# Kernel optimization log

Measured on AMD Instinct MI355X. Metric: run time of the kernel, lower is better.

Reference implementation:

```python
import jax, jax.numpy as jnp
import numpy as np

B, T, NMELS = 2, 2048, 64
D, H, DH, M, L = 256, 4, 64, 384, 4
FF2 = 2 * 4 * D  # GLU doubles the 4*dim hidden


def _layernorm(x, g, b):
    m = x.mean(-1, keepdims=True)
    v = ((x - m) ** 2).mean(-1, keepdims=True)
    return (x - m) * jax.lax.rsqrt(v + 1e-5) * g + b


def _conv(h, w, groups=1, pad='VALID'):
    return jax.lax.conv_general_dilated(h, w, (1, 1), pad, feature_group_count=groups,
                                        dimension_numbers=('NCHW', 'OIHW', 'NCHW'))


def _bn(h, g, b, m, v):
    return (h - m[:, None, None]) * jax.lax.rsqrt(v[:, None, None] + 1e-5) * g[:, None, None] + b[:, None, None]


def setup_inputs():
    key = jax.random.key(0)
    ks = jax.random.split(key, 40)
    def n(i, shape, s):
        return (jax.random.normal(ks[i], shape) * s).astype(jnp.float32)
    z = lambda shape: jnp.zeros(shape, jnp.float32)
    o = lambda shape: jnp.ones(shape, jnp.float32)
    return dict(
        x=n(0, (B, T, NMELS), 1.0),
        conv0_w=n(1, (4, 1, 1, 1), 0.5),
        dw1_w=n(2, (4, 1, 3, 3), 0.3), dw1_b=z(4),
        pw1_w=n(3, (D // 2, 4, 1, 1), 0.5), pw1_b=z(D // 2),
        bn1_g=o(D // 2), bn1_b=z(D // 2), bn1_m=n(4, (D // 2,), 0.05), bn1_v=o(D // 2),
        dw2_w=n(5, (D // 2, 1, 3, 3), 0.3), dw2_b=z(D // 2),
        pw2_w=n(6, (D, D // 2, 1, 1), 0.1), pw2_b=z(D),
        bn2_g=o(D), bn2_b=z(D), bn2_m=n(7, (D,), 0.05), bn2_v=o(D),
        proj_w=n(8, (D, D), 0.06), proj_b=z(D),
        ln0_g=o(D), ln0_b=z(D),
        pos_emb=n(9, (1, T, D), 0.02),
        ln1_g=o((L, D)), ln1_b=z((L, D)),
        wq=n(10, (L, D, D), 0.06), bq=z((L, D)),
        wk=n(11, (L, D, D), 0.06), bk=z((L, D)),
        wv=n(12, (L, D, D), 0.06), bv=z((L, D)),
        wo=n(13, (L, D, D), 0.06), bo=z((L, D)),
        proj_mat=n(14, (L, M, DH), 1.0),
        ln2_g=o((L, D)), ln2_b=z((L, D)),
        ffw1=n(15, (L, D, FF2), 0.06), ffb1=z((L, FF2)),
        ffw2=n(16, (L, FF2 // 2, D), 0.03), ffb2=z((L, D)),
        clf_w1=n(17, (D, D // 2), 0.06), clf_b1=z(D // 2),
        clf_ln_g=o(D // 2), clf_ln_b=z(D // 2),
        clf_w2=n(18, (D // 2, 1), 0.09), clf_b2=z(1),
    )


def reference(x, conv0_w, dw1_w, dw1_b, pw1_w, pw1_b, bn1_g, bn1_b, bn1_m, bn1_v,
              dw2_w, dw2_b, pw2_w, pw2_b, bn2_g, bn2_b, bn2_m, bn2_v,
              proj_w, proj_b, ln0_g, ln0_b, pos_emb,
              ln1_g, ln1_b, wq, bq, wk, bk, wv, bv, wo, bo, proj_mat,
              ln2_g, ln2_b, ffw1, ffb1, ffw2, ffb2,
              clf_w1, clf_b1, clf_ln_g, clf_ln_b, clf_w2, clf_b2):
    pad1 = ((1, 1), (1, 1))
    # conv frontend: [B,T,n_mels] -> [B,1,n_mels,T]
    h = x.transpose(0, 2, 1)[:, None]
    h = _conv(h, conv0_w)
    h = _conv(h, dw1_w, groups=4, pad=pad1) + dw1_b[:, None, None]
    h = _conv(h, pw1_w) + pw1_b[:, None, None]
    h = jax.nn.relu(_bn(h, bn1_g, bn1_b, bn1_m, bn1_v))
    h = _conv(h, dw2_w, groups=D // 2, pad=pad1) + dw2_b[:, None, None]
    h = _conv(h, pw2_w) + pw2_b[:, None, None]
    h = jax.nn.relu(_bn(h, bn2_g, bn2_b, bn2_m, bn2_v))
    h = h.mean(axis=2).transpose(0, 2, 1)  # [B,T,D]
    h = h @ proj_w + proj_b
    h = _layernorm(h, ln0_g, ln0_b) + pos_emb[:, :h.shape[1]]
    # reversible Performer: streams x1 (attn) / x2 (ff), combined by sum
    x1, x2 = h, h
    dn = DH ** -0.25
    for l in range(L):
        a = _layernorm(x2, ln1_g[l], ln1_b[l])
        Bsz, N, _ = a.shape
        q = (a @ wq[l] + bq[l]).reshape(Bsz, N, H, DH).transpose(0, 2, 1, 3)
        k = (a @ wk[l] + bk[l]).reshape(Bsz, N, H, DH).transpose(0, 2, 1, 3)
        v = (a @ wv[l] + bv[l]).reshape(Bsz, N, H, DH).transpose(0, 2, 1, 3)
        # FAVOR+ generalized (ReLU) kernel feature maps, eps=1e-3
        qf = jax.nn.relu(jnp.einsum('bhnd,jd->bhnj', dn * q, proj_mat[l])) + 1e-3
        kf = jax.nn.relu(jnp.einsum('bhnd,jd->bhnj', dn * k, proj_mat[l])) + 1e-3
        d_inv = 1.0 / jnp.einsum('bhnj,bhj->bhn', qf, kf.sum(axis=2))
        ctx = jnp.einsum('bhnj,bhnd->bhjd', kf, v)
        o = jnp.einsum('bhjd,bhnj,bhn->bhnd', ctx, qf, d_inv)
        o = o.transpose(0, 2, 1, 3).reshape(Bsz, N, D)
        x1 = x1 + (o @ wo[l] + bo[l])
        f = _layernorm(x1, ln2_g[l], ln2_b[l])
        u1, u2 = jnp.split(f @ ffw1[l] + ffb1[l], 2, axis=-1)
        x2 = x2 + (jax.nn.gelu(u1, approximate=False) * u2) @ ffw2[l] + ffb2[l]
    h = x1 + x2
    c = jax.nn.relu(_layernorm(h @ clf_w1 + clf_b1, clf_ln_g, clf_ln_b))
    return (c @ clf_w2 + clf_b2)[..., 0]
```

## Files before the change

### kernel.cpp

```cpp
#include <hip/hip_runtime.h>
#include <hip/hip_bf16.h>
#include <math.h>

using bf16 = __hip_bfloat16;
typedef __attribute__((ext_vector_type(8))) short short8;
typedef __attribute__((ext_vector_type(4))) float f32x4;

__device__ __forceinline__ float tof(float x) { return x; }
__device__ __forceinline__ float tof(bf16 x) { return __bfloat162float(x); }
__device__ __forceinline__ float b2f(unsigned short u) {
  union { float f; unsigned int i; } c; c.i = ((unsigned int)u) << 16; return c.f;
}
__device__ __forceinline__ unsigned short f2bu(float v) {
  bf16 h = __float2bfloat16(v);
  return *(unsigned short*)&h;
}
__device__ __forceinline__ void sto1(float* p, float v) { *p = v; }
__device__ __forceinline__ void sto1(bf16* p, float v) { *p = __float2bfloat16(v); }

__device__ __forceinline__ float gelu_exact(float x) {
  return 0.5f * x * (1.f + erff(x * 0.70710678118654752f));
}

__device__ __forceinline__ void llds16(const bf16* g, short* l) {
  __builtin_amdgcn_global_load_lds((const __attribute__((address_space(1))) void*)g,
                                   (__attribute__((address_space(3))) void*)l, 16, 0, 0);
}

__global__ __launch_bounds__(256) void pack_qkv_kernel(
    const float* __restrict__ wq, const float* __restrict__ wk,
    const float* __restrict__ wv, bf16* __restrict__ out)
{
  int idx = blockIdx.x * 256 + threadIdx.x;
  int k = idx & 255;
  int nl = idx >> 8;
  int n = nl % 768, l = nl / 768;
  const float* src = (n < 256) ? wq : (n < 512 ? wk : wv);
  out[idx] = __float2bfloat16(src[(long)l * 65536 + k * 256 + (n & 255)]);
}

__global__ __launch_bounds__(256) void pack_qkvbias_kernel(
    const float* __restrict__ bq, const float* __restrict__ bk,
    const float* __restrict__ bv, float* __restrict__ out)
{
  int i = blockIdx.x * 256 + threadIdx.x;
  if (i >= 3072) return;
  int n = i % 768, l = i / 768;
  const float* src = (n < 256) ? bq : (n < 512 ? bk : bv);
  out[i] = src[l * 256 + (n & 255)];
}

__global__ __launch_bounds__(256) void tconv_kernel(
    const float* __restrict__ in, bf16* __restrict__ out,
    int K, int N, long sin, long sout)
{
  int l = blockIdx.z;
  int idx = blockIdx.x * 256 + threadIdx.x;
  int k = idx % K, n = idx / K;
  out[l * sout + idx] = __float2bfloat16(in[l * sin + (long)k * N + n]);
}

__global__ __launch_bounds__(256) void f2b_kernel(
    const float* __restrict__ in, bf16* __restrict__ out, int n)
{
  int i = blockIdx.x * 256 + threadIdx.x;
  if (i < n) out[i] = __float2bfloat16(in[i]);
}

__global__ __launch_bounds__(256) void zero4_kernel(float* __restrict__ p) {
  int i = (blockIdx.x * 256 + threadIdx.x) * 4;
  float4 z; z.x = 0.f; z.y = 0.f; z.z = 0.f; z.w = 0.f;
  *(float4*)&p[i] = z;
}

__global__ __launch_bounds__(256) void sumb_kernel(
    const float* __restrict__ a, const float* __restrict__ b, bf16* __restrict__ o)
{
  int i = (blockIdx.x * 256 + threadIdx.x) * 4;
  float4 x = *(const float4*)&a[i];
  float4 y = *(const float4*)&b[i];
  ushort4 p;
  p.x = f2bu(x.x + y.x); p.y = f2bu(x.y + y.y);
  p.z = f2bu(x.z + y.z); p.w = f2bu(x.w + y.w);
  *(ushort4*)((unsigned short*)o + i) = p;
}

__global__ __launch_bounds__(256) void front1_kernel(
    const float* __restrict__ x, const float* __restrict__ c0w,
    const float* __restrict__ d1w, const float* __restrict__ d1b,
    const float* __restrict__ p1w, const float* __restrict__ p1b,
    const float* __restrict__ g1, const float* __restrict__ b1,
    const float* __restrict__ m1, const float* __restrict__ v1,
    bf16* __restrict__ A1)
{
  __shared__ float sd[256];
  __shared__ float spw[512];
  __shared__ float ss[128], st[128], sb[128];
  int tid = threadIdx.x;
  int bt = blockIdx.x;
  int b = bt >> 11, t = bt & 2047;
  if (tid < 128) {
    float s = g1[tid] * rsqrtf(v1[tid] + 1e-5f);
    ss[tid] = s;
    st[tid] = b1[tid] - m1[tid] * s;
    sb[tid] = p1b[tid];
#pragma unroll
    for (int c = 0; c < 4; ++c) spw[c * 128 + tid] = p1w[tid * 4 + c];
  }
  {
    int c = tid >> 6, f = tid & 63;
    float cw = c0w[c];
    float acc = d1b[c];
#pragma unroll
    for (int kh = 0; kh < 3; ++kh) {
      int fi = f + kh - 1;
      if (fi < 0 || fi >= 64) continue;
#pragma unroll
      for (int kw = 0; kw < 3; ++kw) {
        int ti = t + kw - 1;
        if (ti < 0 || ti >= 2048) continue;
        acc += d1w[c * 9 + kh * 3 + kw] * cw * x[((long)b * 2048 + ti) * 64 + fi];
      }
    }
    sd[c * 64 + f] = acc;
  }
  __syncthreads();
  long ob = (long)bt * 8192;
  for (int it = 0; it < 32; ++it) {
    int o = it * 256 + tid;
    int f = o >> 7, ci = o & 127;
    float pre = sb[ci];
#pragma unroll
    for (int c = 0; c < 4; ++c) pre = fmaf(spw[c * 128 + ci], sd[c * 64 + f], pre);
    A1[ob + o] = __float2bfloat16(fmaxf(fmaf(ss[ci], pre, st[ci]), 0.f));
  }
}

__global__ __launch_bounds__(256) void convtail_kernel(
    const bf16* __restrict__ A1, const float* __restrict__ w,
    const float* __restrict__ wb, const bf16* __restrict__ w2b,
    const float* __restrict__ pb, const float* __restrict__ g2,
    const float* __restrict__ b2, const float* __restrict__ m2,
    const float* __restrict__ v2, bf16* __restrict__ hconvb)
{
  __shared__ short dw2s[64 * 136];
  __shared__ short Bs[64 * 136];
  __shared__ float red[1024];
  __shared__ float ssc[64], ssh[64];
  int tid = threadIdx.x;
  int lane = tid & 63, wv = tid >> 6;
  int quad = lane >> 4, l15 = lane & 15;
  int rw = (wv >> 1) * 32, cw = (wv & 1) * 32;
  int bt = blockIdx.x, b = bt >> 11, t = bt & 2047;
  int ci4 = (tid & 31) * 4;
  float wreg[9][4], breg[4];
#pragma unroll
  for (int c = 0; c < 4; ++c) {
    breg[c] = wb[ci4 + c];
#pragma unroll
    for (int kk = 0; kk < 9; ++kk) wreg[kk][c] = w[(ci4 + c) * 9 + kk];
  }
  const unsigned short* A1u = (const unsigned short*)A1;
  for (int pass = 0; pass < 8; ++pass) {
    int f = pass * 8 + (tid >> 5);
    float a0 = breg[0], a1 = breg[1], a2 = breg[2], a3 = breg[3];
#pragma unroll
    for (int kh = 0; kh < 3; ++kh) {
      int fi = f + kh - 1;
      if (fi < 0 || fi >= 64) continue;
#pragma unroll
      for (int kw = 0; kw < 3; ++kw) {
        int ti = t + kw - 1;
        if (ti < 0 || ti >= 2048) continue;
        ushort4 u = *(const ushort4*)&A1u[(((long)b * 2048 + ti) * 64 + fi) * 128 + ci4];
        int kk = kh * 3 + kw;
        a0 = fmaf(wreg[kk][0], b2f(u.x), a0);
        a1 = fmaf(wreg[kk][1], b2f(u.y), a1);
        a2 = fmaf(wreg[kk][2], b2f(u.z), a2);
        a3 = fmaf(wreg[kk][3], b2f(u.w), a3);
      }
    }
    ushort4 p; p.x = f2bu(a0); p.y = f2bu(a1); p.z = f2bu(a2); p.w = f2bu(a3);
    *(ushort4*)&dw2s[f * 136 + ci4] = p;
  }
  for (int ct = 0; ct < 4; ++ct) {
    int co0 = ct * 64;
    __syncthreads();
    for (int l2 = 0; l2 < 4; ++l2) {
      int idx = l2 * 256 + tid;
      int row = idx >> 4, koff = (idx & 15) * 8;
      *(short8*)&Bs[row * 136 + koff] =
          *(const short8*)&w2b[(long)(co0 + row) * 128 + koff];
    }
    if (tid < 64) {
      int co = co0 + tid;
      float s = g2[co] * rsqrtf(v2[co] + 1e-5f);
      ssc[tid] = s;
      ssh[tid] = b2[co] - m2[co] * s + s * pb[co];
    }
    __syncthreads();
    f32x4 zv = {0.f, 0.f, 0.f, 0.f};
    f32x4 acc[2][2] = {{zv, zv}, {zv, zv}};
#pragma unroll
    for (int kc = 0; kc < 4; ++kc) {
      short8 a0 = *(const short8*)&dw2s[(rw + l15) * 136 + kc * 32 + quad * 8];
      short8 a1 = *(const short8*)&dw2s[(rw + 16 + l15) * 136 + kc * 32 + quad * 8];
      short8 b0 = *(const short8*)&Bs[(cw + l15) * 136 + kc * 32 + quad * 8];
      short8 b1 = *(const short8*)&Bs[(cw + 16 + l15) * 136 + kc * 32 + quad * 8];
      acc[0][0] = __builtin_amdgcn_mfma_f32_16x16x32_bf16(a0, b0, acc[0][0], 0, 0, 0);
      acc[0][1] = __builtin_amdgcn_mfma_f32_16x16x32_bf16(a0, b1, acc[0][1], 0, 0, 0);
      acc[1][0] = __builtin_amdgcn_mfma_f32_16x16x32_bf16(a1, b0, acc[1][0], 0, 0, 0);
      acc[1][1] = __builtin_amdgcn_mfma_f32_16x16x32_bf16(a1, b1, acc[1][1], 0, 0, 0);
    }
#pragma unroll
    for (int mi = 0; mi < 2; ++mi)
#pragma unroll
      for (int nj = 0; nj < 2; ++nj) {
        int colg = cw + nj * 16 + l15;
        float s = ssc[colg], sh = ssh[colg];
        float sum = 0.f;
#pragma unroll
        for (int r = 0; r < 4; ++r) sum += fmaxf(fmaf(s, acc[mi][nj][r], sh), 0.f);
        int rowgroup = (wv >> 1) * 8 + mi * 4 + quad;
        red[rowgroup * 64 + colg] = sum;
      }
    __syncthreads();
    if (tid < 64) {
      float s = 0.f;
#pragma unroll
      for (int r = 0; r < 16; ++r) s += red[r * 64 + tid];
      hconvb[(long)bt * 256 + co0 + tid] = __float2bfloat16(s * (1.f / 64.f));
    }
  }
}

template <typename CTy, int EPI>
__global__ __launch_bounds__(256) void mgemm_kernel(
    const bf16* __restrict__ A, const bf16* __restrict__ Bt,
    const float* __restrict__ bias, const float* __restrict__ res,
    const float* __restrict__ rowsc, CTy* __restrict__ C, bf16* __restrict__ C2,
    int K, int lda, int ldbt, int ldc,
    long sAb, long sAh, long sBb, long sBh, long sCb, long sCh,
    long sRb, long sRh, int Hdiv, float alpha)
{
  __shared__ short As[4096];
  __shared__ short Bs[4096];
  __shared__ short Bs2[(EPI == 8) ? 4096 : 8];
  int tid = threadIdx.x;
  int lane = tid & 63, w = tid >> 6;
  int quad = lane >> 4, l15 = lane & 15;
  int rw = (w >> 1) * 32, cw = (w & 1) * 32;
  int r0 = blockIdx.x * 64, n0 = blockIdx.y * 64;
  int zb = blockIdx.z / Hdiv, zh = blockIdx.z % Hdiv;
  A += zb * sAb + zh * sAh;
  Bt += zb * sBb + zh * sBh;
  C += zb * sCb + zh * sCh;
  if (res) res += zb * sCb + zh * sCh;
  const float* rsp = (EPI == 3) ? rowsc + zb * sRb + zh * sRh : nullptr;
  f32x4 zv = {0.f, 0.f, 0.f, 0.f};
  f32x4 acc[2][2] = {{zv, zv}, {zv, zv}};
  f32x4 acc2[2][2] = {{zv, zv}, {zv, zv}};
  const bf16* Ag = A + (long)(r0 + (tid >> 2)) * lda + ((tid & 3) * 8);
  const bf16* Bg = Bt + (long)(n0 + (tid >> 2)) * ldbt + ((tid & 3) * 8);
  const bf16* Bg2 = (EPI == 8) ? Bg + sRb : nullptr;
  short* Asd = &As[tid * 8];
  short* Bsd = &Bs[tid * 8];
  short* Bs2d = &Bs2[(EPI == 8) ? tid * 8 : 0];
  for (int k0 = 0; k0 < K; k0 += 64) {
    if (k0) __syncthreads();
    llds16(Ag + k0, Asd);
    llds16(Ag + k0 + 32, Asd + 2048);
    llds16(Bg + k0, Bsd);
    llds16(Bg + k0 + 32, Bsd + 2048);
    if constexpr (EPI == 8) {
      llds16(Bg2 + k0, Bs2d);
      llds16(Bg2 + k0 + 32, Bs2d + 2048);
    }
    __syncthreads();
#pragma unroll
    for (int c = 0; c < 2; ++c) {
      short8 a0 = *(const short8*)&As[c * 2048 + (rw + l15) * 32 + quad * 8];
      short8 a1 = *(const short8*)&As[c * 2048 + (rw + 16 + l15) * 32 + quad * 8];
      short8 b0 = *(const short8*)&Bs[c * 2048 + (cw + l15) * 32 + quad * 8];
      short8 b1 = *(const short8*)&Bs[c * 2048 + (cw + 16 + l15) * 32 + quad * 8];
      acc[0][0] = __builtin_amdgcn_mfma_f32_16x16x32_bf16(a0, b0, acc[0][0], 0, 0, 0);
      acc[0][1] = __builtin_amdgcn_mfma_f32_16x16x32_bf16(a0, b1, acc[0][1], 0, 0, 0);
      acc[1][0] = __builtin_amdgcn_mfma_f32_16x16x32_bf16(a1, b0, acc[1][0], 0, 0, 0);
      acc[1][1] = __builtin_amdgcn_mfma_f32_16x16x32_bf16(a1, b1, acc[1][1], 0, 0, 0);
      if constexpr (EPI == 8) {
        short8 c0 = *(const short8*)&Bs2[c * 2048 + (cw + l15) * 32 + quad * 8];
        short8 c1 = *(const short8*)&Bs2[c * 2048 + (cw + 16 + l15) * 32 + quad * 8];
        acc2[0][0] = __builtin_amdgcn_mfma_f32_16x16x32_bf16(a0, c0, acc2[0][0], 0, 0, 0);
        acc2[0][1] = __builtin_amdgcn_mfma_f32_16x16x32_bf16(a0, c1, acc2[0][1], 0, 0, 0);
        acc2[1][0] = __builtin_amdgcn_mfma_f32_16x16x32_bf16(a1, c0, acc2[1][0], 0, 0, 0);
        acc2[1][1] = __builtin_amdgcn_mfma_f32_16x16x32_bf16(a1, c1, acc2[1][1], 0, 0, 0);
      }
    }
  }
#pragma unroll
  for (int mi = 0; mi < 2; ++mi)
#pragma unroll
    for (int nj = 0; nj < 2; ++nj) {
      int colg = n0 + cw + nj * 16 + l15;
      float bv_ = bias ? bias[colg] : 0.f;
      float bv2 = (EPI == 8) ? bias[colg + 1024] : 0.f;
      int rbase = r0 + rw + mi * 16 + quad * 4;
      float ov[4];
#pragma unroll
      for (int r = 0; r < 4; ++r) {
        float v = acc[mi][nj][r];
        if constexpr (EPI == 0 || EPI == 5) {
          v += bv_;
        } else if constexpr (EPI == 1) {
          v += bv_ + res[(long)(rbase + r) * ldc + colg];
        } else if constexpr (EPI == 2 || EPI == 6) {
          v = fmaxf(v * alpha, 0.f) + 1e-3f;
        } else if constexpr (EPI == 3) {
          v *= rsp[rbase + r];
        } else if constexpr (EPI == 4) {
          v = gelu_exact(v + bv_) * res[(long)(rbase + r) * ldc + colg];
        } else if constexpr (EPI == 8) {
          v = gelu_exact(v + bv_) * (acc2[mi][nj][r] + bv2);
        }
        ov[r] = v;
      }
      if constexpr (EPI == 6) {
        ushort4 p;
        p.x = f2bu(ov[0]); p.y = f2bu(ov[1]); p.z = f2bu(ov[2]); p.w = f2bu(ov[3]);
        *(ushort4*)((unsigned short*)C + (long)colg * ldc + rbase) = p;
      } else if constexpr (EPI == 5) {
        if (colg < 512) {
#pragma unroll
          for (int r = 0; r < 4; ++r) sto1(&C[(long)(rbase + r) * ldc + colg], ov[r]);
        } else {
          int bb = rbase >> 11, t0 = rbase & 2047;
          long off = (((long)bb * 4 + ((colg - 512) >> 6)) * 64 + (colg & 63)) * 2048 + t0;
          ushort4 p;
          p.x = f2bu(ov[0]); p.y = f2bu(ov[1]); p.z = f2bu(ov[2]); p.w = f2bu(ov[3]);
          *(ushort4*)((unsigned short*)C2 + off) = p;
        }
      } else if constexpr (EPI == 7) {
#pragma unroll
        for (int r = 0; r < 4; ++r)
          atomicAdd((float*)&C[(long)(rbase + r) * ldc + colg], ov[r]);
      } else {
#pragma unroll
        for (int r = 0; r < 4; ++r) sto1(&C[(long)(rbase + r) * ldc + colg], ov[r]);
      }
    }
  (void)alpha;
}

template <int DIM, bool RELU, bool ADDPOS, bool DUAL, typename OTy>
__global__ __launch_bounds__(256) void ln_kernel(
    const float* __restrict__ in, const float* __restrict__ g,
    const float* __restrict__ b, const float* __restrict__ pos,
    OTy* __restrict__ out0, float* __restrict__ out1)
{
  constexpr int CH = DIM / 64;
  int row = blockIdx.x * 4 + (threadIdx.x >> 6);
  int lane = threadIdx.x & 63;
  const float* rp = in + (long)row * DIM + lane * CH;
  float v[CH];
#pragma unroll
  for (int i = 0; i < CH; ++i) v[i] = rp[i];
  float s = 0.f;
#pragma unroll
  for (int i = 0; i < CH; ++i) s += v[i];
#pragma unroll
  for (int o = 32; o > 0; o >>= 1) s += __shfl_xor(s, o, 64);
  float mean = s * (1.f / DIM);
  float q = 0.f;
#pragma unroll
  for (int i = 0; i < CH; ++i) { float d = v[i] - mean; q += d * d; }
#pragma unroll
  for (int o = 32; o > 0; o >>= 1) q += __shfl_xor(q, o, 64);
  float rstd = rsqrtf(q * (1.f / DIM) + 1e-5f);
  int t = row & 2047;
#pragma unroll
  for (int i = 0; i < CH; ++i) {
    int c = lane * CH + i;
    float o = (v[i] - mean) * rstd * g[c] + b[c];
    if constexpr (ADDPOS) o += pos[(long)t * DIM + c];
    if constexpr (RELU) o = fmaxf(o, 0.f);
    sto1(&out0[(long)row * DIM + c], o);
    if constexpr (DUAL) out1[(long)row * DIM + c] = o;
  }
}

__global__ __launch_bounds__(256) void rowsum_kernel(
    const bf16* __restrict__ kfT, float* __restrict__ ksum)
{
  int z = blockIdx.x;
  int j = blockIdx.y * 4 + (threadIdx.x >> 6);
  int lane = threadIdx.x & 63;
  const short* base = (const short*)kfT + ((long)z * 384 + j) * 2048;
  float acc = 0.f;
#pragma unroll
  for (int i = 0; i < 4; ++i) {
    short8 v = *(const short8*)&base[i * 512 + lane * 8];
#pragma unroll
    for (int e = 0; e < 8; ++e) acc += b2f((unsigned short)v[e]);
  }
#pragma unroll
  for (int o = 32; o > 0; o >>= 1) acc += __shfl_xor(acc, o, 64);
  if (lane == 0) ksum[z * 384 + j] = acc;
}

__global__ __launch_bounds__(256) void dinv_kernel(
    const bf16* __restrict__ qf, const float* __restrict__ ksum,
    float* __restrict__ dinv)
{
  int z = blockIdx.x;
  int t = blockIdx.y * 4 + (threadIdx.x >> 6);
  int lane = threadIdx.x & 63;
  const bf16* qr = qf + ((long)z * 2048 + t) * 384;
  const float* ks = ksum + z * 384;
  float acc = 0.f;
#pragma unroll
  for (int i = 0; i < 6; ++i) {
    int j = lane + i * 64;
    acc = fmaf(tof(qr[j]), ks[j], acc);
  }
#pragma unroll
  for (int o = 32; o > 0; o >>= 1) acc += __shfl_xor(acc, o, 64);
  if (lane == 0) dinv[z * 2048 + t] = 1.f / acc;
}

__global__ __launch_bounds__(256) void clf2_kernel(
    const float* __restrict__ c2, const float* __restrict__ w,
    const float* __restrict__ b, float* __restrict__ out)
{
  int row = blockIdx.x * 4 + (threadIdx.x >> 6);
  int lane = threadIdx.x & 63;
  const float* rp = c2 + (long)row * 128 + lane * 2;
  float acc = rp[0] * w[lane * 2] + rp[1] * w[lane * 2 + 1];
#pragma unroll
  for (int o = 32; o > 0; o >>= 1) acc += __shfl_xor(acc, o, 64);
  if (lane == 0) out[row] = acc + b[0];
}

extern "C" void kernel_launch(void* const* d_in, const int* in_sizes, int n_in,
                              void* d_out, int out_size, void* d_ws, size_t ws_size,
                              hipStream_t stream)
{
  const float* X    = (const float*)d_in[0];
  const float* c0w  = (const float*)d_in[1];
  const float* d1w  = (const float*)d_in[2];
  const float* d1b  = (const float*)d_in[3];
  const float* p1w  = (const float*)d_in[4];
  const float* p1b  = (const float*)d_in[5];
  const float* g1   = (const float*)d_in[6];
  const float* b1   = (const float*)d_in[7];
  const float* m1   = (const float*)d_in[8];
  const float* v1   = (const float*)d_in[9];
  const float* d2w  = (const float*)d_in[10];
  const float* d2b  = (const float*)d_in[11];
  const float* p2w  = (const float*)d_in[12];
  const float* p2b  = (const float*)d_in[13];
  const float* g2   = (const float*)d_in[14];
  const float* b2   = (const float*)d_in[15];
  const float* m2   = (const float*)d_in[16];
  const float* v2   = (const float*)d_in[17];
  const float* projw= (const float*)d_in[18];
  const float* projb= (const float*)d_in[19];
  const float* ln0g = (const float*)d_in[20];
  const float* ln0b = (const float*)d_in[21];
  const float* pos  = (const float*)d_in[22];
  const float* ln1g = (const float*)d_in[23];
  const float* ln1b = (const float*)d_in[24];
  const float* wq   = (const float*)d_in[25];
  const float* bq   = (const float*)d_in[26];
  const float* wk   = (const float*)d_in[27];
  const float* bk   = (const float*)d_in[28];
  const float* wv   = (const float*)d_in[29];
  const float* bv   = (const float*)d_in[30];
  const float* wo   = (const float*)d_in[31];
  const float* bo   = (const float*)d_in[32];
  const float* pmat = (const float*)d_in[33];
  const float* ln2g = (const float*)d_in[34];
  const float* ln2b = (const float*)d_in[35];
  const float* ffw1 = (const float*)d_in[36];
  const float* ffb1 = (const float*)d_in[37];
  const float* ffw2 = (const float*)d_in[38];
  const float* ffb2 = (const float*)d_in[39];
  const float* cw1  = (const float*)d_in[40];
  const float* cb1  = (const float*)d_in[41];
  const float* clng = (const float*)d_in[42];
  const float* clnb = (const float*)d_in[43];
  const float* cw2  = (const float*)d_in[44];
  const float* cb2  = (const float*)d_in[45];
  (void)in_sizes; (void)n_in; (void)out_size; (void)ws_size;

  float* ws     = (float*)d_ws;
  float* x1     = ws;
  float* x2     = ws + 1048576;
  float* lnb32  = ws + 2097152;
  bf16*  lnb16  = (bf16*)(ws + 3145728);
  bf16*  hconvb = (bf16*)(ws + 3407872);
  bf16*  obufb  = (bf16*)(ws + 3670016);
  bf16*  qkvb   = (bf16*)(ws + 3932160);
  bf16*  vT     = (bf16*)(ws + 5505024);
  bf16*  qf     = (bf16*)(ws + 6029312);
  bf16*  kfT    = (bf16*)(ws + 9175040);
  float* ctx32  = ws + 12320768;
  float* ksum   = ws + 12517376;
  float* dinvp  = ws + 12521472;
  bf16*  ctxb   = (bf16*)(ws + 12537856);
  float* c1     = ws + 12587008;
  float* c2     = ws + 13111296;
  bf16*  gb2    = (bf16*)(ws + 16633856);
  bf16*  A1     = (bf16*)(ws + 3670016);
  bf16*  wqkv_bf= (bf16*)(ws + 20447232);
  float* qkvbias= ws + 20840448;
  bf16*  f1w_bf = (bf16*)(ws + 20843520);
  bf16*  f2w_bf = (bf16*)(ws + 21892096);
  bf16*  wo_bf  = (bf16*)(ws + 22416384);
  bf16*  pm_bf  = (bf16*)(ws + 22547456);
  bf16*  projwT = (bf16*)(ws + 22596608);
  bf16*  cw1T   = (bf16*)(ws + 22629376);
  bf16*  pw2_bf = (bf16*)(ws + 22645760);
  bf16*  sbuf   = qkvb;

  const float dn = 0.35355339059327378f;

  pack_qkv_kernel<<<3072, 256, 0, stream>>>(wq, wk, wv, wqkv_bf);
  pack_qkvbias_kernel<<<12, 256, 0, stream>>>(bq, bk, bv, qkvbias);
  tconv_kernel<<<dim3(2048, 1, 4), 256, 0, stream>>>(ffw1, f1w_bf, 256, 2048, 524288, 524288);
  tconv_kernel<<<dim3(1024, 1, 4), 256, 0, stream>>>(ffw2, f2w_bf, 1024, 256, 262144, 262144);
  tconv_kernel<<<dim3(256, 1, 4), 256, 0, stream>>>(wo, wo_bf, 256, 256, 65536, 65536);
  tconv_kernel<<<dim3(256, 1, 1), 256, 0, stream>>>(projw, projwT, 256, 256, 65536, 65536);
  tconv_kernel<<<dim3(128, 1, 1), 256, 0, stream>>>(cw1, cw1T, 256, 128, 32768, 32768);
  f2b_kernel<<<384, 256, 0, stream>>>(pmat, pm_bf, 98304);
  f2b_kernel<<<128, 256, 0, stream>>>(p2w, pw2_bf, 32768);

  front1_kernel<<<4096, 256, 0, stream>>>(X, c0w, d1w, d1b, p1w, p1b, g1, b1, m1, v1, A1);
  convtail_kernel<<<4096, 256, 0, stream>>>(A1, d2w, d2b, pw2_bf, p2b, g2, b2, m2, v2, hconvb);

  mgemm_kernel<float, 0><<<dim3(64, 4, 1), 256, 0, stream>>>(
      hconvb, projwT, projb, nullptr, nullptr, lnb32, nullptr,
      256, 256, 256, 256, 0, 0, 0, 0, 0, 0, 0, 0, 1, 1.f);
  ln_kernel<256, false, true, true, float><<<1024, 256, 0, stream>>>(
      lnb32, ln0g, ln0b, pos, x1, x2);

  for (int l = 0; l < 4; ++l) {
    const bf16* wqkv_l = wqkv_bf + (size_t)l * 196608;
    const float* qb_l  = qkvbias + l * 768;
    const bf16* pm_l   = pm_bf + (size_t)l * 24576;
    const bf16* wo_l   = wo_bf + (size_t)l * 65536;
    const float* bov   = bo + l * 256;
    const bf16* f1w_l  = f1w_bf + (size_t)l * 524288;
    const float* f1b_l = ffb1 + l * 2048;
    const bf16* f2w_l  = f2w_bf + (size_t)l * 262144;
    const float* f2b_l = ffb2 + l * 256;

    ln_kernel<256, false, false, false, bf16><<<1024, 256, 0, stream>>>(
        x2, ln1g + l * 256, ln1b + l * 256, nullptr, lnb16, nullptr);
    mgemm_kernel<bf16, 5><<<dim3(64, 12, 1), 256, 0, stream>>>(
        lnb16, wqkv_l, qb_l, nullptr, nullptr, qkvb, vT,
        256, 256, 256, 768, 0, 0, 0, 0, 0, 0, 0, 0, 1, 1.f);
    mgemm_kernel<bf16, 2><<<dim3(32, 6, 8), 256, 0, stream>>>(
        qkvb, pm_l, nullptr, nullptr, nullptr, qf, nullptr,
        64, 768, 64, 384, 1572864, 64, 0, 0, 3145728, 786432, 0, 0, 4, dn);
    mgemm_kernel<bf16, 6><<<dim3(32, 6, 8), 256, 0, stream>>>(
        qkvb + 256, pm_l, nullptr, nullptr, nullptr, kfT, nullptr,
        64, 768, 64, 2048, 1572864, 64, 0, 0, 6291456, 1572864, 0, 0, 4, dn);
    rowsum_kernel<<<dim3(8, 96), 256, 0, stream>>>(kfT, ksum);
    dinv_kernel<<<dim3(8, 512), 256, 0, stream>>>(qf, ksum, dinvp);
    zero4_kernel<<<192, 256, 0, stream>>>(ctx32);
    mgemm_kernel<float, 7><<<dim3(1, 6, 64), 256, 0, stream>>>(
        vT, kfT, nullptr, nullptr, nullptr, ctx32, nullptr,
        256, 2048, 2048, 384, 131072, 256, 786432, 256, 24576, 0, 0, 0, 8, 1.f);
    f2b_kernel<<<768, 256, 0, stream>>>(ctx32, ctxb, 196608);
    mgemm_kernel<bf16, 3><<<dim3(32, 1, 8), 256, 0, stream>>>(
        qf, ctxb, nullptr, nullptr, dinvp, obufb, nullptr,
        384, 384, 384, 256, 3145728, 786432, 98304, 24576, 524288, 64, 8192, 2048, 4, 1.f);
    mgemm_kernel<float, 1><<<dim3(64, 4, 1), 256, 0, stream>>>(
        obufb, wo_l, bov, x1, nullptr, x1, nullptr,
        256, 256, 256, 256, 0, 0, 0, 0, 0, 0, 0, 0, 1, 1.f);
    ln_kernel<256, false, false, false, bf16><<<1024, 256, 0, stream>>>(
        x1, ln2g + l * 256, ln2b + l * 256, nullptr, lnb16, nullptr);
    mgemm_kernel<bf16, 8><<<dim3(64, 16, 1), 256, 0, stream>>>(
        lnb16, f1w_l, f1b_l, nullptr, nullptr, gb2, nullptr,
        256, 256, 256, 1024, 0, 0, 0, 0, 0, 0, 262144, 0, 1, 1.f);
    mgemm_kernel<float, 1><<<dim3(64, 4, 1), 256, 0, stream>>>(
        gb2, f2w_l, f2b_l, x2, nullptr, x2, nullptr,
        1024, 1024, 1024, 256, 0, 0, 0, 0, 0, 0, 0, 0, 1, 1.f);
  }

  sumb_kernel<<<1024, 256, 0, stream>>>(x1, x2, sbuf);
  mgemm_kernel<float, 0><<<dim3(64, 2, 1), 256, 0, stream>>>(
      sbuf, cw1T, cb1, nullptr, nullptr, c1, nullptr,
      256, 256, 256, 128, 0, 0, 0, 0, 0, 0, 0, 0, 1, 1.f);
  ln_kernel<128, true, false, false, float><<<1024, 256, 0, stream>>>(
      c1, clng, clnb, nullptr, c2, nullptr);
  clf2_kernel<<<1024, 256, 0, stream>>>(c2, cw2, cb2, (float*)d_out);
}
```

Baseline: 680.9 us.

## Fuse FAVOR+ q/k feature maps with key-sum and widen convtail depthwise vectors

The separate q and k feature-map GEMM launches and the rowsum kernel are replaced by a single favor_kernel. It computes both maps over a doubled z grid and accumulates the key sums with atomics, which assumes the widened zero kernel also clears ksum. The convtail depthwise stage now handles 8 channels per thread with 16-byte loads and stores, and gets a launch-bounds occupancy hint. This cuts launches and the re-read of kfT, at the cost of float atomics with nondeterministic ordering and higher register use in convtail.

```diff
diff --git a/kernel.cpp b/kernel.cpp
--- a/kernel.cpp
+++ b/kernel.cpp
@@ -136,7 +136,7 @@
   }
 }
 
-__global__ __launch_bounds__(256) void convtail_kernel(
+__global__ __launch_bounds__(256, 4) void convtail_kernel(
     const bf16* __restrict__ A1, const float* __restrict__ w,
     const float* __restrict__ wb, const bf16* __restrict__ w2b,
     const float* __restrict__ pb, const float* __restrict__ g2,
@@ -152,18 +152,20 @@
   int quad = lane >> 4, l15 = lane & 15;
   int rw = (wv >> 1) * 32, cw = (wv & 1) * 32;
   int bt = blockIdx.x, b = bt >> 11, t = bt & 2047;
-  int ci4 = (tid & 31) * 4;
-  float wreg[9][4], breg[4];
-#pragma unroll
-  for (int c = 0; c < 4; ++c) {
-    breg[c] = wb[ci4 + c];
-#pragma unroll
-    for (int kk = 0; kk < 9; ++kk) wreg[kk][c] = w[(ci4 + c) * 9 + kk];
+  int ci8 = (tid & 15) * 8;
+  float wreg[9][8], breg[8];
+#pragma unroll
+  for (int c = 0; c < 8; ++c) {
+    breg[c] = wb[ci8 + c];
+#pragma unroll
+    for (int kk = 0; kk < 9; ++kk) wreg[kk][c] = w[(ci8 + c) * 9 + kk];
   }
   const unsigned short* A1u = (const unsigned short*)A1;
-  for (int pass = 0; pass < 8; ++pass) {
-    int f = pass * 8 + (tid >> 5);
-    float a0 = breg[0], a1 = breg[1], a2 = breg[2], a3 = breg[3];
+  for (int pass = 0; pass < 4; ++pass) {
+    int f = pass * 16 + (tid >> 4);
+    float a[8];
+#pragma unroll
+    for (int c = 0; c < 8; ++c) a[c] = breg[c];
 #pragma unroll
     for (int kh = 0; kh < 3; ++kh) {
       int fi = f + kh - 1;
@@ -172,16 +174,17 @@
       for (int kw = 0; kw < 3; ++kw) {
         int ti = t + kw - 1;
         if (ti < 0 || ti >= 2048) continue;
-        ushort4 u = *(const ushort4*)&A1u[(((long)b * 2048 + ti) * 64 + fi) * 128 + ci4];
+        short8 u = *(const short8*)&A1u[(((long)b * 2048 + ti) * 64 + fi) * 128 + ci8];
         int kk = kh * 3 + kw;
-        a0 = fmaf(wreg[kk][0], b2f(u.x), a0);
-        a1 = fmaf(wreg[kk][1], b2f(u.y), a1);
-        a2 = fmaf(wreg[kk][2], b2f(u.z), a2);
-        a3 = fmaf(wreg[kk][3], b2f(u.w), a3);
+#pragma unroll
+        for (int c = 0; c < 8; ++c)
+          a[c] = fmaf(wreg[kk][c], b2f((unsigned short)u[c]), a[c]);
       }
     }
-    ushort4 p; p.x = f2bu(a0); p.y = f2bu(a1); p.z = f2bu(a2); p.w = f2bu(a3);
-    *(ushort4*)&dw2s[f * 136 + ci4] = p;
+    short8 p;
+#pragma unroll
+    for (int c = 0; c < 8; ++c) p[c] = (short)f2bu(a[c]);
+    *(short8*)&dw2s[f * 136 + ci8] = p;
   }
   for (int ct = 0; ct < 4; ++ct) {
     int co0 = ct * 64;
@@ -232,6 +235,68 @@
       hconvb[(long)bt * 256 + co0 + tid] = __float2bfloat16(s * (1.f / 64.f));
     }
   }
+}
+
+__global__ __launch_bounds__(256) void favor_kernel(
+    const bf16* __restrict__ qkvb, const bf16* __restrict__ pm,
+    bf16* __restrict__ qf, bf16* __restrict__ kfT, float* __restrict__ ksum,
+    float dn)
+{
+  __shared__ short As[4096];
+  __shared__ short Bs[4096];
+  int tid = threadIdx.x;
+  int lane = tid & 63, w = tid >> 6;
+  int quad = lane >> 4, l15 = lane & 15;
+  int rw = (w >> 1) * 32, cw = (w & 1) * 32;
+  int r0 = blockIdx.x * 64, n0 = blockIdx.y * 64;
+  int z16 = blockIdx.z;
+  bool isK = z16 >= 8;
+  int z = z16 & 7, zb = z >> 2, zh = z & 3;
+  const bf16* A = qkvb + (isK ? 256 : 0) + (long)zb * 1572864 + zh * 64;
+  f32x4 zv = {0.f, 0.f, 0.f, 0.f};
+  f32x4 acc[2][2] = {{zv, zv}, {zv, zv}};
+  const bf16* Ag = A + (long)(r0 + (tid >> 2)) * 768 + ((tid & 3) * 8);
+  const bf16* Bg = pm + (long)(n0 + (tid >> 2)) * 64 + ((tid & 3) * 8);
+  llds16(Ag, &As[tid * 8]);
+  llds16(Ag + 32, &As[tid * 8 + 2048]);
+  llds16(Bg, &Bs[tid * 8]);
+  llds16(Bg + 32, &Bs[tid * 8 + 2048]);
+  __syncthreads();
+#pragma unroll
+  for (int c = 0; c < 2; ++c) {
+    short8 a0 = *(const short8*)&As[c * 2048 + (rw + l15) * 32 + quad * 8];
+    short8 a1 = *(const short8*)&As[c * 2048 + (rw + 16 + l15) * 32 + quad * 8];
+    short8 b0 = *(const short8*)&Bs[c * 2048 + (cw + l15) * 32 + quad * 8];
+    short8 b1 = *(const short8*)&Bs[c * 2048 + (cw + 16 + l15) * 32 + quad * 8];
+    acc[0][0] = __builtin_amdgcn_mfma_f32_16x16x32_bf16(a0, b0, acc[0][0], 0, 0, 0);
+    acc[0][1] = __builtin_amdgcn_mfma_f32_16x16x32_bf16(a0, b1, acc[0][1], 0, 0, 0);
+    acc[1][0] = __builtin_amdgcn_mfma_f32_16x16x32_bf16(a1, b0, acc[1][0], 0, 0, 0);
+    acc[1][1] = __builtin_amdgcn_mfma_f32_16x16x32_bf16(a1, b1, acc[1][1], 0, 0, 0);
+  }
+  bf16* qfz = qf + (long)zb * 3145728 + (long)zh * 786432;
+  unsigned short* kfz = (unsigned short*)kfT + (long)zb * 3145728 + (long)zh * 786432;
+  float* ksz = ksum + z * 384;
+#pragma unroll
+  for (int mi = 0; mi < 2; ++mi)
+#pragma unroll
+    for (int nj = 0; nj < 2; ++nj) {
+      int colg = n0 + cw + nj * 16 + l15;
+      int rbase = r0 + rw + mi * 16 + quad * 4;
+      float ov[4];
+#pragma unroll
+      for (int r = 0; r < 4; ++r)
+        ov[r] = fmaxf(acc[mi][nj][r] * dn, 0.f) + 1e-3f;
+      if (!isK) {
+#pragma unroll
+        for (int r = 0; r < 4; ++r)
+          qfz[(long)(rbase + r) * 384 + colg] = __float2bfloat16(ov[r]);
+      } else {
+        ushort4 p;
+        p.x = f2bu(ov[0]); p.y = f2bu(ov[1]); p.z = f2bu(ov[2]); p.w = f2bu(ov[3]);
+        *(ushort4*)&kfz[(long)colg * 2048 + rbase] = p;
+        atomicAdd(&ksz[colg], ov[0] + ov[1] + ov[2] + ov[3]);
+      }
+    }
 }
 
 template <typename CTy, int EPI>
@@ -313,22 +378,14 @@
           v += bv_;
         } else if constexpr (EPI == 1) {
           v += bv_ + res[(long)(rbase + r) * ldc + colg];
-        } else if constexpr (EPI == 2 || EPI == 6) {
-          v = fmaxf(v * alpha, 0.f) + 1e-3f;
         } else if constexpr (EPI == 3) {
           v *= rsp[rbase + r];
-        } else if constexpr (EPI == 4) {
-          v = gelu_exact(v + bv_) * res[(long)(rbase + r) * ldc + colg];
         } else if constexpr (EPI == 8) {
           v = gelu_exact(v + bv_) * (acc2[mi][nj][r] + bv2);
         }
         ov[r] = v;
       }
-      if constexpr (EPI == 6) {
-        ushort4 p;
-        p.x = f2bu(ov[0]); p.y = f2bu(ov[1]); p.z = f2bu(ov[2]); p.w = f2bu(ov[3]);
-        *(ushort4*)((unsigned short*)C + (long)colg * ldc + rbase) = p;
-      } else if constexpr (EPI == 5) {
+      if constexpr (EPI == 5) {
         if (colg < 512) {
 #pragma unroll
           for (int r = 0; r < 4; ++r) sto1(&C[(long)(rbase + r) * ldc + colg], ov[r]);
@@ -386,25 +443,6 @@
     sto1(&out0[(long)row * DIM + c], o);
     if constexpr (DUAL) out1[(long)row * DIM + c] = o;
   }
-}
-
-__global__ __launch_bounds__(256) void rowsum_kernel(
-    const bf16* __restrict__ kfT, float* __restrict__ ksum)
-{
-  int z = blockIdx.x;
-  int j = blockIdx.y * 4 + (threadIdx.x >> 6);
-  int lane = threadIdx.x & 63;
-  const short* base = (const short*)kfT + ((long)z * 384 + j) * 2048;
-  float acc = 0.f;
-#pragma unroll
-  for (int i = 0; i < 4; ++i) {
-    short8 v = *(const short8*)&base[i * 512 + lane * 8];
-#pragma unroll
-    for (int e = 0; e < 8; ++e) acc += b2f((unsigned short)v[e]);
-  }
-#pragma unroll
-  for (int o = 32; o > 0; o >>= 1) acc += __shfl_xor(acc, o, 64);
-  if (lane == 0) ksum[z * 384 + j] = acc;
 }
 
 __global__ __launch_bounds__(256) void dinv_kernel(
@@ -559,15 +597,10 @@
     mgemm_kernel<bf16, 5><<<dim3(64, 12, 1), 256, 0, stream>>>(
         lnb16, wqkv_l, qb_l, nullptr, nullptr, qkvb, vT,
         256, 256, 256, 768, 0, 0, 0, 0, 0, 0, 0, 0, 1, 1.f);
-    mgemm_kernel<bf16, 2><<<dim3(32, 6, 8), 256, 0, stream>>>(
-        qkvb, pm_l, nullptr, nullptr, nullptr, qf, nullptr,
-        64, 768, 64, 384, 1572864, 64, 0, 0, 3145728, 786432, 0, 0, 4, dn);
-    mgemm_kernel<bf16, 6><<<dim3(32, 6, 8), 256, 0, stream>>>(
-        qkvb + 256, pm_l, nullptr, nullptr, nullptr, kfT, nullptr,
-        64, 768, 64, 2048, 1572864, 64, 0, 0, 6291456, 1572864, 0, 0, 4, dn);
-    rowsum_kernel<<<dim3(8, 96), 256, 0, stream>>>(kfT, ksum);
+    zero4_kernel<<<196, 256, 0, stream>>>(ctx32);
+    favor_kernel<<<dim3(32, 6, 16), 256, 0, stream>>>(
+        qkvb, pm_l, qf, kfT, ksum, dn);
     dinv_kernel<<<dim3(8, 512), 256, 0, stream>>>(qf, ksum, dinvp);
-    zero4_kernel<<<192, 256, 0, stream>>>(ctx32);
     mgemm_kernel<float, 7><<<dim3(1, 6, 64), 256, 0, stream>>>(
         vT, kfT, nullptr, nullptr, nullptr, ctx32, nullptr,
         256, 2048, 2048, 384, 131072, 256, 786432, 256, 24576, 0, 0, 0, 8, 1.f);
```

Result: slower. 927.6 us (+36.2%).
